# Optimization experiments

Hardware: AMD Instinct MI355X
Metric: run time of the kernel (lower is better)

Reference implementation:

```python
import jax, jax.numpy as jnp
import numpy as np

N_HEADS = 16


def setup_inputs() -> dict:
    key = jax.random.key(0)
    k_x, k_len, k_pos, k_attn, k_proj = jax.random.split(key, 5)
    B, W, c, C = 4, 256, 32, 1024
    x = jax.random.normal(k_x, (B, W, c, C), dtype=jnp.float32)
    # ragged word lengths in [1, c]; left-aligned padding mask as in pad()
    lengths = jax.random.randint(k_len, (B, W), 1, c + 1)
    attention_mask = (jnp.arange(c)[None, None, :] < lengths[:, :, None]).astype(jnp.int32)
    pos_emb = jax.random.normal(k_pos, (W, C), dtype=jnp.float32) * 0.02
    attn_w = jax.random.normal(k_attn, (C, 3 * C), dtype=jnp.float32) * (C ** -0.5)
    proj_w = jax.random.normal(k_proj, (C, C), dtype=jnp.float32) * (C ** -0.5)
    return {"x": x, "attention_mask": attention_mask, "pos_emb": pos_emb,
            "attn_w": attn_w, "proj_w": proj_w}


def reference(x, attention_mask, pos_emb, attn_w, proj_w):
    # first_time=True path of CharAttention.forward (eval mode: dropout = identity)
    B, W, c, C = x.shape
    H = N_HEADS
    hd = C // H
    last_ix = jnp.sum(attention_mask, axis=2) - 1          # [B, W]

    qkv = jnp.einsum('bwce,ef->bwcf', x, attn_w)            # [B, W, c, 3C]
    q, k, v = jnp.split(qkv, 3, axis=-1)
    # [B, W, c, C] -> [B, W, H, c, hd]
    def to_heads(t):
        return t.reshape(B, W, c, H, hd).transpose(0, 1, 3, 2, 4)
    q, k, v = to_heads(q), to_heads(k), to_heads(v)

    scale = 1.0 / jnp.sqrt(jnp.asarray(hd, dtype=x.dtype))
    scores = jnp.einsum('bwhqd,bwhkd->bwhqk', q, k) * scale  # [B, W, H, c, c]
    causal = jnp.tril(jnp.ones((c, c), dtype=bool))
    scores = jnp.where(causal[None, None, None], scores, jnp.finfo(x.dtype).min)
    attn = jax.nn.softmax(scores, axis=-1)
    o = jnp.einsum('bwhqk,bwhkd->bwhqd', attn, v)            # [B, W, H, c, hd]
    o = o.transpose(0, 1, 3, 2, 4).reshape(B, W, c, C)       # [B, W, c, C]

    # gather the last real-character position of each word
    idx = last_ix[:, :, None, None]                          # [B, W, 1, 1]
    gathered = jnp.take_along_axis(o, idx, axis=2)[:, :, 0, :]  # [B, W, C]

    out = gathered + pos_emb[None, :, :]
    out = jnp.einsum('bwe,ef->bwf', out, proj_w)
    return out
```

## Files before the change

### kernel.cpp

```cpp
#include <hip/hip_runtime.h>
#include <hip/hip_bf16.h>
#include <stdint.h>

typedef __attribute__((ext_vector_type(8))) short short8;
typedef __attribute__((ext_vector_type(4))) float floatx4;

#define GPTR(p) (const __attribute__((address_space(1))) void*)(p)
#define LPTR(p) (__attribute__((address_space(3))) void*)(p)

__device__ __forceinline__ ushort f2bf(float f) {
    union { float f; uint32_t u; } v; v.f = f;
    uint32_t u = v.u;
    uint32_t r = (u + 0x7FFFu + ((u >> 16) & 1u)) >> 16;
    return (ushort)r;
}
__device__ __forceinline__ float bf2f(ushort b) {
    union { uint32_t u; float f; } v; v.u = ((uint32_t)b) << 16;
    return v.f;
}

__global__ void prep_kernel(const float* __restrict__ attn_w, const float* __restrict__ proj_w,
                            const float* __restrict__ x, const int* __restrict__ mask,
                            ushort* __restrict__ wqT, ushort* __restrict__ wk,
                            ushort* __restrict__ wvT, ushort* __restrict__ wpT,
                            ushort* __restrict__ xq) {
    __shared__ float tile[32][33];
    __shared__ int t_sh;
    const int bx = blockIdx.x, by = blockIdx.y;
    const int tid = threadIdx.x;

    if (bx >= 128) {
        int bw = (bx - 128) * 32 + by;
        if (tid < 32) {
            int s = mask[bw * 32 + tid];
            #pragma unroll
            for (int off = 16; off; off >>= 1) s += __shfl_xor(s, off);
            if (tid == 0) t_sh = s - 1;
        }
        __syncthreads();
        int t = t_sh;
        float4 v = ((const float4*)(x + ((size_t)bw * 32 + t) * 1024))[tid];
        ushort4 o;
        o.x = f2bf(v.x); o.y = f2bf(v.y); o.z = f2bf(v.z); o.w = f2bf(v.w);
        ((ushort4*)(xq + (size_t)bw * 1024))[tid] = o;
        return;
    }

    const int tx = tid & 31, ty = tid >> 5;
    const int r0 = by * 32;
    if (bx >= 96) {
        int c0 = (bx - 96) * 32;
        for (int i = ty; i < 32; i += 8)
            wk[(size_t)(r0 + i) * 1024 + c0 + tx] =
                f2bf(attn_w[(size_t)(r0 + i) * 3072 + 1024 + c0 + tx]);
        return;
    }
    const float* src; ushort* dst; int N, csrc0, c0;
    if (bx < 32)      { src = attn_w; dst = wqT; N = 3072; c0 = bx * 32;        csrc0 = c0; }
    else if (bx < 64) { src = attn_w; dst = wvT; N = 3072; c0 = (bx - 32) * 32; csrc0 = 2048 + c0; }
    else              { src = proj_w; dst = wpT; N = 1024; c0 = (bx - 64) * 32; csrc0 = c0; }
    for (int i = ty; i < 32; i += 8)
        tile[i][tx] = src[(size_t)(r0 + i) * N + csrc0 + tx];
    __syncthreads();
    for (int i = ty; i < 32; i += 8)
        dst[(size_t)(c0 + i) * 1024 + r0 + tx] = f2bf(tile[tx][i]);
}

__global__ __launch_bounds__(256)
void gemm64sk_kernel(const ushort* __restrict__ A, const ushort* __restrict__ Bt,
                     float* __restrict__ Cpart) {
    __shared__ ushort As[64 * 32];
    __shared__ ushort Bs[64 * 32];

    const int bm = blockIdx.x, bn = blockIdx.y, z = blockIdx.z;
    const int kofs = z * 256;

    const int tid  = threadIdx.x;
    const int wave = tid >> 6;
    const int lane = tid & 63;
    const int wm = wave & 1, wn = wave >> 1;
    const int quad = lane >> 4, l15 = lane & 15;

    floatx4 acc[2][2] = {};

    const int srow = wave * 16 + (lane >> 2);
    const int kcol = (lane & 3) * 8;

    for (int kt = 0; kt < 256; kt += 32) {
        const ushort* gA = A  + (size_t)(bm * 64 + srow) * 1024 + kofs + kt + kcol;
        const ushort* gB = Bt + (size_t)(bn * 64 + srow) * 1024 + kofs + kt + kcol;
        ushort* lA = As + (wave * 16) * 32;
        ushort* lB = Bs + (wave * 16) * 32;
        __builtin_amdgcn_global_load_lds(GPTR(gA), LPTR(lA), 16, 0, 0);
        __builtin_amdgcn_global_load_lds(GPTR(gB), LPTR(lB), 16, 0, 0);
        __syncthreads();

        short8 af[2], bf[2];
        #pragma unroll
        for (int i = 0; i < 2; ++i)
            af[i] = *(const short8*)&As[(wm * 32 + i * 16 + l15) * 32 + quad * 8];
        #pragma unroll
        for (int j = 0; j < 2; ++j)
            bf[j] = *(const short8*)&Bs[(wn * 32 + j * 16 + l15) * 32 + quad * 8];
        #pragma unroll
        for (int i = 0; i < 2; ++i)
            #pragma unroll
            for (int j = 0; j < 2; ++j)
                acc[i][j] = __builtin_amdgcn_mfma_f32_16x16x32_bf16(af[i], bf[j], acc[i][j], 0, 0, 0);
        __syncthreads();
    }

    #pragma unroll
    for (int i = 0; i < 2; ++i) {
        #pragma unroll
        for (int j = 0; j < 2; ++j) {
            int r0 = bm * 64 + wm * 32 + i * 16 + quad * 4;
            int c  = bn * 64 + wn * 32 + j * 16 + l15;
            #pragma unroll
            for (int r = 0; r < 4; ++r)
                Cpart[(size_t)z * 1048576 + (size_t)(r0 + r) * 1024 + c] = acc[i][j][r];
        }
    }
}

template <bool OUT_BF16>
__global__ void combine4_kernel(const float* __restrict__ P, void* __restrict__ C) {
    int i = blockIdx.x * 256 + threadIdx.x;
    const float4* p = (const float4*)P;
    float4 a = p[i], b = p[i + 262144], c = p[i + 524288], d = p[i + 786432];
    float4 s;
    s.x = a.x + b.x + c.x + d.x;
    s.y = a.y + b.y + c.y + d.y;
    s.z = a.z + b.z + c.z + d.z;
    s.w = a.w + b.w + c.w + d.w;
    if (OUT_BF16) {
        ushort4 o;
        o.x = f2bf(s.x); o.y = f2bf(s.y); o.z = f2bf(s.z); o.w = f2bf(s.w);
        ((ushort4*)C)[i] = o;
    } else {
        ((float4*)C)[i] = s;
    }
}

template <bool OUT_BF16>
__global__ __launch_bounds__(256)
void gemm128_kernel(const ushort* __restrict__ A, int lda, long sA,
                    const ushort* __restrict__ Bt, int ldb, long sB,
                    void* __restrict__ C, int ldc, long sC, int K) {
    __shared__ ushort As[128 * 32];
    __shared__ ushort Bs[128 * 32];

    const int bm = blockIdx.x, bn = blockIdx.y, z = blockIdx.z;
    A  += (size_t)z * sA;
    Bt += (size_t)z * sB;

    const int tid  = threadIdx.x;
    const int wave = tid >> 6;
    const int lane = tid & 63;
    const int wm = wave & 1, wn = wave >> 1;
    const int quad = lane >> 4, l15 = lane & 15;

    floatx4 acc[4][4] = {};

    const int arow = bm * 128 + wave * 16 + (lane >> 2);
    const int brow = bn * 128 + wave * 16 + (lane >> 2);
    const int kcol = (lane & 3) * 8;

    for (int kt = 0; kt < K; kt += 32) {
        #pragma unroll
        for (int iss = 0; iss < 2; ++iss) {
            const ushort* gA = A  + (size_t)(arow + iss * 64) * lda + kt + kcol;
            const ushort* gB = Bt + (size_t)(brow + iss * 64) * ldb + kt + kcol;
            ushort* lA = As + (iss * 64 + wave * 16) * 32;
            ushort* lB = Bs + (iss * 64 + wave * 16) * 32;
            __builtin_amdgcn_global_load_lds(GPTR(gA), LPTR(lA), 16, 0, 0);
            __builtin_amdgcn_global_load_lds(GPTR(gB), LPTR(lB), 16, 0, 0);
        }
        __syncthreads();

        short8 af[4], bf[4];
        #pragma unroll
        for (int i = 0; i < 4; ++i)
            af[i] = *(const short8*)&As[(wm * 64 + i * 16 + l15) * 32 + quad * 8];
        #pragma unroll
        for (int j = 0; j < 4; ++j)
            bf[j] = *(const short8*)&Bs[(wn * 64 + j * 16 + l15) * 32 + quad * 8];
        #pragma unroll
        for (int i = 0; i < 4; ++i)
            #pragma unroll
            for (int j = 0; j < 4; ++j)
                acc[i][j] = __builtin_amdgcn_mfma_f32_16x16x32_bf16(af[i], bf[j], acc[i][j], 0, 0, 0);
        __syncthreads();
    }

    #pragma unroll
    for (int i = 0; i < 4; ++i) {
        #pragma unroll
        for (int j = 0; j < 4; ++j) {
            int r0 = bm * 128 + wm * 64 + i * 16 + quad * 4;
            int c  = bn * 128 + wn * 64 + j * 16 + l15;
            #pragma unroll
            for (int r = 0; r < 4; ++r) {
                float v = acc[i][j][r];
                size_t idx = (size_t)z * sC + (size_t)(r0 + r) * ldc + c;
                if (OUT_BF16) ((ushort*)C)[idx] = f2bf(v);
                else          ((float*) C)[idx] = v;
            }
        }
    }
}

template <bool OUT_BF16, bool ADD_POS>
__global__ __launch_bounds__(256)
void gemm64_kernel(const ushort* __restrict__ A, int lda, long sA,
                   const ushort* __restrict__ Bt, int ldb, long sB,
                   void* __restrict__ C, int ldc, int cColPerZ, int K,
                   const float* __restrict__ pos) {
    __shared__ ushort As[64 * 32];
    __shared__ ushort Bs[64 * 32];

    const int bm = blockIdx.x, bn = blockIdx.y, z = blockIdx.z;
    A  += (size_t)z * sA;
    Bt += (size_t)z * sB;

    const int tid  = threadIdx.x;
    const int wave = tid >> 6;
    const int lane = tid & 63;
    const int wm = wave & 1, wn = wave >> 1;
    const int quad = lane >> 4, l15 = lane & 15;

    floatx4 acc[2][2] = {};

    const int srow = wave * 16 + (lane >> 2);
    const int kcol = (lane & 3) * 8;

    for (int kt = 0; kt < K; kt += 32) {
        const ushort* gA = A  + (size_t)(bm * 64 + srow) * lda + kt + kcol;
        const ushort* gB = Bt + (size_t)(bn * 64 + srow) * ldb + kt + kcol;
        ushort* lA = As + (wave * 16) * 32;
        ushort* lB = Bs + (wave * 16) * 32;
        __builtin_amdgcn_global_load_lds(GPTR(gA), LPTR(lA), 16, 0, 0);
        __builtin_amdgcn_global_load_lds(GPTR(gB), LPTR(lB), 16, 0, 0);
        __syncthreads();

        short8 af[2], bf[2];
        #pragma unroll
        for (int i = 0; i < 2; ++i)
            af[i] = *(const short8*)&As[(wm * 32 + i * 16 + l15) * 32 + quad * 8];
        #pragma unroll
        for (int j = 0; j < 2; ++j)
            bf[j] = *(const short8*)&Bs[(wn * 32 + j * 16 + l15) * 32 + quad * 8];
        #pragma unroll
        for (int i = 0; i < 2; ++i)
            #pragma unroll
            for (int j = 0; j < 2; ++j)
                acc[i][j] = __builtin_amdgcn_mfma_f32_16x16x32_bf16(af[i], bf[j], acc[i][j], 0, 0, 0);
        __syncthreads();
    }

    #pragma unroll
    for (int i = 0; i < 2; ++i) {
        #pragma unroll
        for (int j = 0; j < 2; ++j) {
            int r0 = bm * 64 + wm * 32 + i * 16 + quad * 4;
            int cc = z * cColPerZ + bn * 64 + wn * 32 + j * 16 + l15;
            #pragma unroll
            for (int r = 0; r < 4; ++r) {
                float v = acc[i][j][r];
                if (ADD_POS) v += pos[(size_t)((r0 + r) & 255) * 1024 + cc];
                size_t idx = (size_t)(r0 + r) * ldc + cc;
                if (OUT_BF16) ((ushort*)C)[idx] = f2bf(v);
                else          ((float*) C)[idx] = v;
            }
        }
    }
}

__global__ __launch_bounds__(256)
void attn2_kernel(const float* __restrict__ x, const int* __restrict__ mask,
                  const ushort* __restrict__ U, ushort* __restrict__ Z) {
    __shared__ ushort Xs[32 * 264];
    __shared__ ushort Us[16 * 264];
    __shared__ float  Sp[2][16][16];
    __shared__ float  Ss[16 * 36];
    __shared__ float  Ps[32 * 16];
    __shared__ int    t_sh;

    const int bw = blockIdx.x;
    const int tid = threadIdx.x;
    const int wave = tid >> 6, lane = tid & 63;
    const int quad = lane >> 4, l15 = lane & 15;

    if (tid < 32) {
        int s = mask[bw * 32 + tid];
        #pragma unroll
        for (int off = 16; off; off >>= 1) s += __shfl_xor(s, off);
        if (tid == 0) t_sh = s - 1;
    }
    __syncthreads();
    const int t = t_sh;

    const int m  = wave & 1;
    const int kh = wave >> 1;
    floatx4 acc = {0.f, 0.f, 0.f, 0.f};

    const float4* xsrc = (const float4*)(x + (size_t)bw * 32768);
    const ushort* ubase = U + (size_t)bw * 16384;

    for (int c = 0; c < 4; ++c) {
        int nx4 = (t + 1) * 64;
        for (int i = tid; i < nx4; i += 256) {
            int j = i >> 6, c4 = i & 63;
            float4 v = xsrc[j * 256 + c * 64 + c4];
            ushort4 o; o.x = f2bf(v.x); o.y = f2bf(v.y); o.z = f2bf(v.z); o.w = f2bf(v.w);
            *(ushort4*)&Xs[j * 264 + c4 * 4] = o;
        }
        for (int i = tid; i < 16 * 32; i += 256) {
            int h = i >> 5, c8 = i & 31;
            *(short8*)&Us[h * 264 + c8 * 8] = *(const short8*)&ubase[h * 1024 + c * 256 + c8 * 8];
        }
        __syncthreads();
        #pragma unroll
        for (int ks = 0; ks < 4; ++ks) {
            short8 a = *(const short8*)&Xs[(m * 16 + l15) * 264 + kh * 128 + ks * 32 + quad * 8];
            short8 b = *(const short8*)&Us[l15 * 264 + kh * 128 + ks * 32 + quad * 8];
            acc = __builtin_amdgcn_mfma_f32_16x16x32_bf16(a, b, acc, 0, 0, 0);
        }
        __syncthreads();
    }

    if (kh == 1) {
        #pragma unroll
        for (int r = 0; r < 4; ++r) Sp[m][quad * 4 + r][l15] = acc[r];
    }
    __syncthreads();
    if (kh == 0) {
        #pragma unroll
        for (int r = 0; r < 4; ++r)
            Ss[l15 * 36 + m * 16 + quad * 4 + r] =
                (acc[r] + Sp[m][quad * 4 + r][l15]) * 0.125f;
    }
    __syncthreads();

    if (wave == 0) {
        float s[8]; float mx = -1e30f;
        #pragma unroll
        for (int r = 0; r < 8; ++r) {
            int j = quad * 8 + r;
            float v = Ss[l15 * 36 + j];
            v = (j <= t) ? v : -1e30f;
            s[r] = v; mx = fmaxf(mx, v);
        }
        mx = fmaxf(mx, __shfl_xor(mx, 16));
        mx = fmaxf(mx, __shfl_xor(mx, 32));
        float l = 0.f;
        #pragma unroll
        for (int r = 0; r < 8; ++r) { s[r] = __expf(s[r] - mx); l += s[r]; }
        l += __shfl_xor(l, 16);
        l += __shfl_xor(l, 32);
        float inv = 1.f / l;
        #pragma unroll
        for (int r = 0; r < 8; ++r)
            Ps[(quad * 8 + r) * 16 + l15] = s[r] * inv;
    }
    __syncthreads();

    float z[16][4];
    #pragma unroll
    for (int h = 0; h < 16; ++h)
        #pragma unroll
        for (int cc = 0; cc < 4; ++cc) z[h][cc] = 0.f;
    for (int j = 0; j <= t; ++j) {
        float4 p0 = *(const float4*)&Ps[j * 16 + 0];
        float4 p1 = *(const float4*)&Ps[j * 16 + 4];
        float4 p2 = *(const float4*)&Ps[j * 16 + 8];
        float4 p3 = *(const float4*)&Ps[j * 16 + 12];
        float pr[16] = {p0.x, p0.y, p0.z, p0.w, p1.x, p1.y, p1.z, p1.w,
                        p2.x, p2.y, p2.z, p2.w, p3.x, p3.y, p3.z, p3.w};
        float4 xv = xsrc[j * 256 + tid];
        float xf[4] = {xv.x, xv.y, xv.z, xv.w};
        #pragma unroll
        for (int h = 0; h < 16; ++h)
            #pragma unroll
            for (int cc = 0; cc < 4; ++cc)
                z[h][cc] += pr[h] * xf[cc];
    }
    const int e0 = tid * 4;
    #pragma unroll
    for (int h = 0; h < 16; ++h) {
        ushort4 o;
        o.x = f2bf(z[h][0]); o.y = f2bf(z[h][1]);
        o.z = f2bf(z[h][2]); o.w = f2bf(z[h][3]);
        *(ushort4*)&Z[(size_t)bw * 16384 + h * 1024 + e0] = o;
    }
}

extern "C" void kernel_launch(void* const* d_in, const int* in_sizes, int n_in,
                              void* d_out, int out_size, void* d_ws, size_t ws_size,
                              hipStream_t stream) {
    const float* x        = (const float*)d_in[0];
    const int*   mask     = (const int*)  d_in[1];
    const float* pos_emb  = (const float*)d_in[2];
    const float* attn_w   = (const float*)d_in[3];
    const float* proj_w   = (const float*)d_in[4];
    float*       out      = (float*)d_out;

    const long MB2 = 1048576;

    char* ws = (char*)d_ws;
    size_t off = 0;
    ushort* U_bf  = (ushort*)(ws + off); off += (size_t)16 * MB2 * 2;
    ushort* Z_bf  = (ushort*)(ws + off); off += (size_t)16 * MB2 * 2;
    float*  qpart = (float*) (ws + off); off += (size_t)4 * MB2 * 4;
    float*  opart = (float*) (ws + off); off += (size_t)4 * MB2 * 4;
    ushort* wqT   = (ushort*)(ws + off); off += MB2 * 2;
    ushort* wk    = (ushort*)(ws + off); off += MB2 * 2;
    ushort* wvT   = (ushort*)(ws + off); off += MB2 * 2;
    ushort* wpT   = (ushort*)(ws + off); off += MB2 * 2;
    ushort* xq_bf = (ushort*)(ws + off); off += MB2 * 2;
    ushort* q_bf  = (ushort*)(ws + off); off += MB2 * 2;
    ushort* y_bf  = (ushort*)(ws + off); off += MB2 * 2;

    prep_kernel<<<dim3(160, 32), 256, 0, stream>>>(attn_w, proj_w, x, mask,
                                                   wqT, wk, wvT, wpT, xq_bf);

    gemm64sk_kernel<<<dim3(16, 16, 4), 256, 0, stream>>>(xq_bf, wqT, qpart);
    combine4_kernel<true><<<1024, 256, 0, stream>>>(qpart, (void*)q_bf);

    gemm128_kernel<true><<<dim3(8, 8, 16), 256, 0, stream>>>(
        q_bf, 1024, 64, wk, 1024, 64, (void*)U_bf, 16384, 1024, 64);

    attn2_kernel<<<1024, 256, 0, stream>>>(x, mask, U_bf, Z_bf);

    gemm64_kernel<true, true><<<dim3(16, 1, 16), 256, 0, stream>>>(
        Z_bf, 16384, 1024, wvT, 1024, 65536, (void*)y_bf, 1024, 64, 1024, pos_emb);

    gemm64sk_kernel<<<dim3(16, 16, 4), 256, 0, stream>>>(y_bf, wpT, opart);
    combine4_kernel<false><<<1024, 256, 0, stream>>>(opart, (void*)out);
}
```

Before: 279.8 us.

## Load MFMA operands directly from global, dropping LDS staging in U-gemm and attention

The per-head U gemm (K=64) now loads both operand fragments straight from global memory into registers and runs all MFMAs with no LDS staging or barriers. The attention score kernel likewise reads x rows and U directly from global per lane, converting to bf16 in registers, skips loads for rows past the last valid character, and removes the shared tiles and the four sync-separated chunks. This cuts LDS traffic and barrier stalls. In exchange, global accesses are less coalesced (each lane reads 16-32 bytes per row) and register pressure rises.

```diff
diff --git a/kernel.cpp b/kernel.cpp
--- a/kernel.cpp
+++ b/kernel.cpp
@@ -142,56 +142,36 @@
     }
 }
 
-template <bool OUT_BF16>
 __global__ __launch_bounds__(256)
-void gemm128_kernel(const ushort* __restrict__ A, int lda, long sA,
-                    const ushort* __restrict__ Bt, int ldb, long sB,
-                    void* __restrict__ C, int ldc, long sC, int K) {
-    __shared__ ushort As[128 * 32];
-    __shared__ ushort Bs[128 * 32];
-
+void gemmu_kernel(const ushort* __restrict__ A, const ushort* __restrict__ Bt,
+                  ushort* __restrict__ C) {
     const int bm = blockIdx.x, bn = blockIdx.y, z = blockIdx.z;
-    A  += (size_t)z * sA;
-    Bt += (size_t)z * sB;
-
     const int tid  = threadIdx.x;
     const int wave = tid >> 6;
     const int lane = tid & 63;
     const int wm = wave & 1, wn = wave >> 1;
     const int quad = lane >> 4, l15 = lane & 15;
 
+    const ushort* Ab = A  + (size_t)(bm * 128 + wm * 64 + l15) * 1024 + z * 64 + quad * 8;
+    const ushort* Bb = Bt + (size_t)(bn * 128 + wn * 64 + l15) * 1024 + z * 64 + quad * 8;
+
+    short8 af[4][2], bfr[4][2];
+    #pragma unroll
+    for (int i = 0; i < 4; ++i)
+        #pragma unroll
+        for (int kk = 0; kk < 2; ++kk) {
+            af[i][kk]  = *(const short8*)(Ab + (size_t)(i * 16) * 1024 + kk * 32);
+            bfr[i][kk] = *(const short8*)(Bb + (size_t)(i * 16) * 1024 + kk * 32);
+        }
+
     floatx4 acc[4][4] = {};
-
-    const int arow = bm * 128 + wave * 16 + (lane >> 2);
-    const int brow = bn * 128 + wave * 16 + (lane >> 2);
-    const int kcol = (lane & 3) * 8;
-
-    for (int kt = 0; kt < K; kt += 32) {
-        #pragma unroll
-        for (int iss = 0; iss < 2; ++iss) {
-            const ushort* gA = A  + (size_t)(arow + iss * 64) * lda + kt + kcol;
-            const ushort* gB = Bt + (size_t)(brow + iss * 64) * ldb + kt + kcol;
-            ushort* lA = As + (iss * 64 + wave * 16) * 32;
-            ushort* lB = Bs + (iss * 64 + wave * 16) * 32;
-            __builtin_amdgcn_global_load_lds(GPTR(gA), LPTR(lA), 16, 0, 0);
-            __builtin_amdgcn_global_load_lds(GPTR(gB), LPTR(lB), 16, 0, 0);
-        }
-        __syncthreads();
-
-        short8 af[4], bf[4];
+    #pragma unroll
+    for (int kk = 0; kk < 2; ++kk)
         #pragma unroll
         for (int i = 0; i < 4; ++i)
-            af[i] = *(const short8*)&As[(wm * 64 + i * 16 + l15) * 32 + quad * 8];
-        #pragma unroll
-        for (int j = 0; j < 4; ++j)
-            bf[j] = *(const short8*)&Bs[(wn * 64 + j * 16 + l15) * 32 + quad * 8];
-        #pragma unroll
-        for (int i = 0; i < 4; ++i)
             #pragma unroll
             for (int j = 0; j < 4; ++j)
-                acc[i][j] = __builtin_amdgcn_mfma_f32_16x16x32_bf16(af[i], bf[j], acc[i][j], 0, 0, 0);
-        __syncthreads();
-    }
+                acc[i][j] = __builtin_amdgcn_mfma_f32_16x16x32_bf16(af[i][kk], bfr[j][kk], acc[i][j], 0, 0, 0);
 
     #pragma unroll
     for (int i = 0; i < 4; ++i) {
@@ -200,12 +180,8 @@
             int r0 = bm * 128 + wm * 64 + i * 16 + quad * 4;
             int c  = bn * 128 + wn * 64 + j * 16 + l15;
             #pragma unroll
-            for (int r = 0; r < 4; ++r) {
-                float v = acc[i][j][r];
-                size_t idx = (size_t)z * sC + (size_t)(r0 + r) * ldc + c;
-                if (OUT_BF16) ((ushort*)C)[idx] = f2bf(v);
-                else          ((float*) C)[idx] = v;
-            }
+            for (int r = 0; r < 4; ++r)
+                C[(size_t)(r0 + r) * 16384 + (size_t)z * 1024 + c] = f2bf(acc[i][j][r]);
         }
     }
 }
@@ -279,8 +255,6 @@
 __global__ __launch_bounds__(256)
 void attn2_kernel(const float* __restrict__ x, const int* __restrict__ mask,
                   const ushort* __restrict__ U, ushort* __restrict__ Z) {
-    __shared__ ushort Xs[32 * 264];
-    __shared__ ushort Us[16 * 264];
     __shared__ float  Sp[2][16][16];
     __shared__ float  Ss[16 * 36];
     __shared__ float  Ps[32 * 16];
@@ -302,31 +276,26 @@
 
     const int m  = wave & 1;
     const int kh = wave >> 1;
+    const int row = m * 16 + l15;
+    const bool live = (row <= t);
+
+    const float*  xrow = x + ((size_t)bw * 32 + row) * 1024 + kh * 512 + quad * 8;
+    const ushort* urow = U + (size_t)bw * 16384 + (size_t)l15 * 1024 + kh * 512 + quad * 8;
+
     floatx4 acc = {0.f, 0.f, 0.f, 0.f};
-
-    const float4* xsrc = (const float4*)(x + (size_t)bw * 32768);
-    const ushort* ubase = U + (size_t)bw * 16384;
-
-    for (int c = 0; c < 4; ++c) {
-        int nx4 = (t + 1) * 64;
-        for (int i = tid; i < nx4; i += 256) {
-            int j = i >> 6, c4 = i & 63;
-            float4 v = xsrc[j * 256 + c * 64 + c4];
-            ushort4 o; o.x = f2bf(v.x); o.y = f2bf(v.y); o.z = f2bf(v.z); o.w = f2bf(v.w);
-            *(ushort4*)&Xs[j * 264 + c4 * 4] = o;
-        }
-        for (int i = tid; i < 16 * 32; i += 256) {
-            int h = i >> 5, c8 = i & 31;
-            *(short8*)&Us[h * 264 + c8 * 8] = *(const short8*)&ubase[h * 1024 + c * 256 + c8 * 8];
-        }
-        __syncthreads();
-        #pragma unroll
-        for (int ks = 0; ks < 4; ++ks) {
-            short8 a = *(const short8*)&Xs[(m * 16 + l15) * 264 + kh * 128 + ks * 32 + quad * 8];
-            short8 b = *(const short8*)&Us[l15 * 264 + kh * 128 + ks * 32 + quad * 8];
-            acc = __builtin_amdgcn_mfma_f32_16x16x32_bf16(a, b, acc, 0, 0, 0);
-        }
-        __syncthreads();
+    #pragma unroll
+    for (int ks = 0; ks < 16; ++ks) {
+        short8 a = (short8)0;
+        if (live) {
+            float4 v0 = *(const float4*)(xrow + ks * 32);
+            float4 v1 = *(const float4*)(xrow + ks * 32 + 4);
+            a[0] = (short)f2bf(v0.x); a[1] = (short)f2bf(v0.y);
+            a[2] = (short)f2bf(v0.z); a[3] = (short)f2bf(v0.w);
+            a[4] = (short)f2bf(v1.x); a[5] = (short)f2bf(v1.y);
+            a[6] = (short)f2bf(v1.z); a[7] = (short)f2bf(v1.w);
+        }
+        short8 b = *(const short8*)(urow + ks * 32);
+        acc = __builtin_amdgcn_mfma_f32_16x16x32_bf16(a, b, acc, 0, 0, 0);
     }
 
     if (kh == 1) {
@@ -365,6 +334,7 @@
     }
     __syncthreads();
 
+    const float4* xsrc = (const float4*)(x + (size_t)bw * 32768);
     float z[16][4];
     #pragma unroll
     for (int h = 0; h < 16; ++h)
@@ -427,8 +397,7 @@
     gemm64sk_kernel<<<dim3(16, 16, 4), 256, 0, stream>>>(xq_bf, wqT, qpart);
     combine4_kernel<true><<<1024, 256, 0, stream>>>(qpart, (void*)q_bf);
 
-    gemm128_kernel<true><<<dim3(8, 8, 16), 256, 0, stream>>>(
-        q_bf, 1024, 64, wk, 1024, 64, (void*)U_bf, 16384, 1024, 64);
+    gemmu_kernel<<<dim3(8, 8, 16), 256, 0, stream>>>(q_bf, wk, U_bf);
 
     attn2_kernel<<<1024, 256, 0, stream>>>(x, mask, U_bf, Z_bf);
 
```

Result: no change. 276.5 us (-1.2%).
